# Optimization experiments

Measured on AMD Instinct MI355X. Metric: run time of the kernel, lower is better.

## Reference

```python
import jax, jax.numpy as jnp
import numpy as np

N_AGENTS = 8
N_ACTIONS = 16
SAMPLE = 16
STATE_DIM = 256
EMBED = 256
IN_DIM = N_AGENTS * N_ACTIONS + STATE_DIM  # 384


def setup_inputs() -> dict:
    key = jax.random.key(0)
    ks = jax.random.split(key, 12)
    bs, t = 32, 32
    s = 0.05
    return {
        "states": jax.random.normal(ks[0], (bs, t, STATE_DIM), jnp.float32),
        "agent_qs": jax.random.normal(ks[1], (bs, t, N_AGENTS, N_ACTIONS), jnp.float32),
        "W1": jax.random.normal(ks[2], (IN_DIM, EMBED), jnp.float32) * s,
        "b1": jnp.zeros((EMBED,), jnp.float32),
        "W2": jax.random.normal(ks[3], (EMBED, EMBED), jnp.float32) * s,
        "b2": jnp.zeros((EMBED,), jnp.float32),
        "W3": jax.random.normal(ks[4], (EMBED, 1), jnp.float32) * s,
        "b3": jnp.zeros((1,), jnp.float32),
        "Vw1": jax.random.normal(ks[5], (STATE_DIM, EMBED), jnp.float32) * s,
        "Vb1": jnp.zeros((EMBED,), jnp.float32),
        "Vw2": jax.random.normal(ks[6], (EMBED, 1), jnp.float32) * s,
        "Vb2": jnp.zeros((1,), jnp.float32),
    }


def reference(states, agent_qs, W1, b1, W2, b2, W3, b3, Vw1, Vb1, Vw2, Vb2):
    bs, t = states.shape[0], states.shape[1]
    B = bs * t
    A, NA, S, sd = N_AGENTS, N_ACTIONS, SAMPLE, STATE_DIM
    st = states.reshape(B, sd)
    qs = agent_qs.reshape(B, A, NA)

    # --- sample grand coalitions (random permutation per (B,S) row) ---
    perm_key = jax.random.key(42)
    u = jax.random.uniform(perm_key, (B, S, A))
    pos = jnp.argsort(u, axis=-1)          # grand_coalitions_pos: agent i -> position pos[i]
    inv = jnp.argsort(pos, axis=-1)        # grand_coalitions: position j -> agent inv[j]

    indiv = jax.nn.one_hot(pos, A, dtype=st.dtype)                         # (B,S,A,A)
    subcoal = (jnp.arange(A)[None, None, None, :] <= pos[..., None]).astype(st.dtype)
    no_i = subcoal - indiv                                                 # coalition members excl. self

    # reorder agent qs along position dim: reordered[b,s,j,:] = qs[b, inv[b,s,j], :]
    reordered = jnp.take_along_axis(
        jnp.broadcast_to(qs[:, None], (B, S, A, NA)), inv[..., None], axis=2)

    # (B,S,A,A,NA): detach contribution of other coalition members
    coal = (jax.lax.stop_gradient(reordered[:, :, None] * no_i[..., None])
            + reordered[:, :, None] * indiv[..., None])

    x = coal.reshape(B * S * A, A * NA)
    stx = jnp.broadcast_to(st[:, None, None], (B, S, A, sd)).reshape(B * S * A, sd)
    inp = jnp.concatenate([stx, x], axis=1)

    h = jax.nn.relu(inp @ W1 + b1)
    h = jax.nn.relu(h @ W2 + b2)
    advs = h @ W3 + b3
    v = jax.nn.relu(stx @ Vw1 + Vb1) @ Vw2 + Vb2

    marginal = (advs + v).reshape(B, S, A)
    shapley = marginal.mean(axis=1)        # mean over samples
    return shapley.reshape(bs, t, A)
```

## Files before the change

kernel.cpp:

```cpp
#include <hip/hip_runtime.h>


#define A_N   8
#define NA_N  16
#define S_N   16
#define SD    256
#define EMB   256
#define B_TOT 1024

typedef __bf16 bf16x8 __attribute__((ext_vector_type(8)));
typedef float  f32x4  __attribute__((ext_vector_type(4)));

__device__ __forceinline__ f32x4 splat4(float v) {
  f32x4 x; x[0] = v; x[1] = v; x[2] = v; x[3] = v; return x;
}
__device__ __forceinline__ bf16x8 zero8() {
  bf16x8 z;
#pragma unroll
  for (int j = 0; j < 8; ++j) z[j] = (__bf16)0.0f;
  return z;
}

__device__ __forceinline__ float jax_uniform(unsigned idx) {
  const unsigned ks0 = 0u, ks1 = 42u, ks2 = 0x1BD11BDAu ^ 42u;
  unsigned x0 = 0u + ks0;
  unsigned x1 = idx + ks1;
#define TF_RND(r) { x0 += x1; x1 = (x1 << (r)) | (x1 >> (32 - (r))); x1 ^= x0; }
  TF_RND(13) TF_RND(15) TF_RND(26) TF_RND(6)  x0 += ks1; x1 += ks2 + 1u;
  TF_RND(17) TF_RND(29) TF_RND(16) TF_RND(24) x0 += ks2; x1 += ks0 + 2u;
  TF_RND(13) TF_RND(15) TF_RND(26) TF_RND(6)  x0 += ks0; x1 += ks1 + 3u;
  TF_RND(17) TF_RND(29) TF_RND(16) TF_RND(24) x0 += ks1; x1 += ks2 + 4u;
  TF_RND(13) TF_RND(15) TF_RND(26) TF_RND(6)  x0 += ks2; x1 += ks0 + 5u;
#undef TF_RND
  const unsigned bits = x0 ^ x1;
  return __uint_as_float((bits >> 9) | 0x3F800000u) - 1.0f;
}

__global__ __launch_bounds__(256) void prep_pack_kernel(
    const float* __restrict__ states, const float* __restrict__ W1,
    const float* __restrict__ b1, const float* __restrict__ Vw1,
    const float* __restrict__ Vb1, const float* __restrict__ Vw2,
    const float* __restrict__ Vb2, const float* __restrict__ W2,
    float* __restrict__ sW, float* __restrict__ vout,
    __bf16* __restrict__ W1b_bf, __bf16* __restrict__ W2_bf) {
  __shared__ float st_l[2][SD];
  __shared__ float red_l[2][4];

  if (blockIdx.x >= 512) {
    const int ts = (blockIdx.x - 512) * 256 + threadIdx.x;
    if (ts < 4096) {
      const int t = ts >> 10, rem = ts & 1023, u = rem >> 6, Lp = rem & 63;
      const int qp = Lp >> 4, l15p = Lp & 15;
#pragma unroll
      for (int j = 0; j < 8; ++j) {
        const int k = t * 32 + qp * 8 + j, nn = u * 16 + l15p;
        W1b_bf[ts * 8 + j] = (__bf16)W1[(SD + k) * EMB + nn];
      }
    } else {
      const int ts2 = ts - 4096;
      const int t = ts2 >> 10, rem = ts2 & 1023, u = rem >> 6, Lp = rem & 63;
      const int qp = Lp >> 4, l15p = Lp & 15;
#pragma unroll
      for (int j = 0; j < 8; ++j) {
        const int k = t * 32 + qp * 8 + j, nn = u * 16 + l15p;
        W2_bf[ts2 * 8 + j] = (__bf16)W2[k * EMB + nn];
      }
    }
    return;
  }

  const int b0 = blockIdx.x * 2;
  const int n = threadIdx.x;

#pragma unroll
  for (int i = 0; i < 2; ++i) st_l[i][n] = states[(b0 + i) * SD + n];
  __syncthreads();

  float aS[2], aV[2];
  const float b1n = b1[n], vb1n = Vb1[n];
#pragma unroll
  for (int i = 0; i < 2; ++i) { aS[i] = b1n; aV[i] = vb1n; }

#pragma unroll 8
  for (int k = 0; k < SD; ++k) {
    const float wv = W1[k * EMB + n];
    const float vw = Vw1[k * EMB + n];
#pragma unroll
    for (int i = 0; i < 2; ++i) {
      const float s = st_l[i][k];
      aS[i] = fmaf(s, wv, aS[i]);
      aV[i] = fmaf(s, vw, aV[i]);
    }
  }
#pragma unroll
  for (int i = 0; i < 2; ++i) sW[(b0 + i) * EMB + n] = aS[i];

  const float vw2 = Vw2[n];
#pragma unroll
  for (int i = 0; i < 2; ++i) {
    float c = fmaxf(aV[i], 0.f) * vw2;
#pragma unroll
    for (int off = 32; off; off >>= 1) c += __shfl_down(c, off);
    if ((n & 63) == 0) red_l[i][n >> 6] = c;
  }
  __syncthreads();
  if (n < 2)
    vout[b0 + n] = red_l[n][0] + red_l[n][1] + red_l[n][2] + red_l[n][3] + Vb2[0];
}

__global__ __launch_bounds__(256, 4) void main_kernel(
    const float* __restrict__ agent_qs, const float* __restrict__ b2g,
    const float* __restrict__ W3, const float* __restrict__ b3,
    const float* __restrict__ sW, const float* __restrict__ vv,
    const __bf16* __restrict__ W1b_bf, const __bf16* __restrict__ W2_bf,
    float* __restrict__ out) {
  __shared__ bf16x8 h1_l[32 * 64];
  __shared__ __attribute__((aligned(16))) __bf16 qs_bf[A_N * NA_N];
  __shared__ float u_l[128];
  __shared__ int   inv_l[128];
  __shared__ int   pos_l[128];
  __shared__ float adv_part[4][64];
  __shared__ float marg_l[128];

  const int b = blockIdx.x;
  const int n = threadIdx.x;
  const int w = n >> 6, L = n & 63, q = L >> 4, l15 = L & 15;
  const int s7 = l15 & 7;
  const int sl = l15 >> 3;
  const int jq = q >> 1;
  const int na0 = (q & 1) * 8;
  const int Lsw = L ^ ((L >> 3) & 3);

  if (n < 128) {
    qs_bf[n] = (__bf16)agent_qs[b * 128 + n];
    u_l[n] = jax_uniform((unsigned)(b * 128 + n));
  }
  __syncthreads();

  if (n < 128) {
    const int s = n >> 3, a = n & 7;
    const float u = u_l[n];
    int r = 0;
#pragma unroll
    for (int a2 = 0; a2 < A_N; ++a2) {
      const float u2 = u_l[s * 8 + a2];
      r += (u2 < u || (u2 == u && a2 < a)) ? 1 : 0;
    }
    inv_l[n] = r;
    pos_l[s * 8 + r] = a;
  }
  __syncthreads();

  const bool diag_on = (jq <= sl);

#pragma unroll 1
  for (int p = 0; p < 2; ++p) {
    const int invbase = (p * 8 + s7) * 8;

#pragma unroll 1
    for (int nh = 0; nh < 2; ++nh) {
      f32x4 acc[4][2];
#pragma unroll
      for (int i = 0; i < 2; ++i) {
        const float sv = sW[b * EMB + (w * 4 + nh * 2 + i) * 16 + l15];
#pragma unroll
        for (int mt = 0; mt < 4; ++mt) acc[mt][i] = splat4(sv);
      }
#pragma unroll
      for (int t = 0; t < 4; ++t) {
        const int ag = inv_l[invbase + 2 * t + jq];
        const bf16x8 afb = *(const bf16x8*)&qs_bf[ag * NA_N + na0];
        const bf16x8 afd = diag_on ? afb : zero8();
        bf16x8 bfr[2];
#pragma unroll
        for (int i = 0; i < 2; ++i)
          bfr[i] = *(const bf16x8*)
              &W1b_bf[((t * 16 + w * 4 + nh * 2 + i) * 64 + L) * 8];
#pragma unroll
        for (int mt = 0; mt < 4; ++mt) {
          if (mt < t) continue;
#pragma unroll
          for (int i = 0; i < 2; ++i)
            acc[mt][i] = __builtin_amdgcn_mfma_f32_16x16x32_bf16(
                (mt == t) ? afd : afb, bfr[i], acc[mt][i], 0, 0, 0);
        }
      }
      __bf16* h1e = (__bf16*)h1_l;
#pragma unroll
      for (int i = 0; i < 2; ++i) {
        const int X = w * 4 + nh * 2 + i;
        const int hi = (X & 1) * 2 + sl;
        const int xr = (q >> 1) | ((hi & 1) << 1);
#pragma unroll
        for (int mt = 0; mt < 4; ++mt) {
          const int ub = ((X >> 1) * 4 + mt) * 64 + (hi << 4);
#pragma unroll
          for (int r = 0; r < 4; ++r) {
            const float v = fmaxf(acc[mt][i][r], 0.f);
            const int u = ub + ((q * 4 + r) ^ xr);
            h1e[u * 8 + s7] = (__bf16)v;
          }
        }
      }
    }
    __syncthreads();

    float psum[4][4];
#pragma unroll
    for (int mt = 0; mt < 4; ++mt)
#pragma unroll
      for (int r = 0; r < 4; ++r) psum[mt][r] = 0.f;

#pragma unroll 1
    for (int nh = 0; nh < 2; ++nh) {
      f32x4 acc[4][2];
#pragma unroll
      for (int i = 0; i < 2; ++i) {
        const float bv = b2g[(w * 4 + nh * 2 + i) * 16 + l15];
#pragma unroll
        for (int mt = 0; mt < 4; ++mt) acc[mt][i] = splat4(bv);
      }
#pragma unroll 2
      for (int t = 0; t < 8; ++t) {
        bf16x8 bfr[2];
#pragma unroll
        for (int i = 0; i < 2; ++i)
          bfr[i] = *(const bf16x8*)
              &W2_bf[((t * 16 + w * 4 + nh * 2 + i) * 64 + L) * 8];
#pragma unroll
        for (int mt = 0; mt < 4; ++mt) {
          const bf16x8 af = h1_l[(t * 4 + mt) * 64 + Lsw];
#pragma unroll
          for (int i = 0; i < 2; ++i)
            acc[mt][i] = __builtin_amdgcn_mfma_f32_16x16x32_bf16(
                af, bfr[i], acc[mt][i], 0, 0, 0);
        }
      }
#pragma unroll
      for (int i = 0; i < 2; ++i) {
        const float w3v = W3[(w * 4 + nh * 2 + i) * 16 + l15];
#pragma unroll
        for (int mt = 0; mt < 4; ++mt)
#pragma unroll
          for (int r = 0; r < 4; ++r)
            psum[mt][r] = fmaf(fmaxf(acc[mt][i][r], 0.f), w3v, psum[mt][r]);
      }
    }

#pragma unroll
    for (int mt = 0; mt < 4; ++mt) {
#pragma unroll
      for (int r = 0; r < 4; ++r) {
        float sum = psum[mt][r];
#pragma unroll
        for (int off = 1; off < 16; off <<= 1) sum += __shfl_xor(sum, off);
        if (l15 == 0) adv_part[w][mt * 16 + q * 4 + r] = sum;
      }
    }
    __syncthreads();
    if (n < 64)
      marg_l[p * 64 + n] = adv_part[0][n] + adv_part[1][n] +
                           adv_part[2][n] + adv_part[3][n];
    __syncthreads();
  }

  if (n < A_N) {
    float sh = 0.f;
#pragma unroll
    for (int s = 0; s < S_N; ++s) {
      const int pr = pos_l[s * 8 + n];
      sh += marg_l[((s >> 3) << 6) + pr * 8 + (s & 7)];
    }
    out[b * A_N + n] = sh * (1.f / 16.f) + b3[0] + vv[b];
  }
}

extern "C" void kernel_launch(void* const* d_in, const int* in_sizes, int n_in,
                              void* d_out, int out_size, void* d_ws,
                              size_t ws_size, hipStream_t stream) {
  const float* states   = (const float*)d_in[0];
  const float* agent_qs = (const float*)d_in[1];
  const float* W1       = (const float*)d_in[2];
  const float* b1       = (const float*)d_in[3];
  const float* W2       = (const float*)d_in[4];
  const float* b2       = (const float*)d_in[5];
  const float* W3       = (const float*)d_in[6];
  const float* b3       = (const float*)d_in[7];
  const float* Vw1      = (const float*)d_in[8];
  const float* Vb1      = (const float*)d_in[9];
  const float* Vw2      = (const float*)d_in[10];
  const float* Vb2      = (const float*)d_in[11];
  float* out = (float*)d_out;

  char* ws = (char*)d_ws;
  float*  sW     = (float*)(ws);
  float*  vv     = (float*)(ws + 1048576);
  __bf16* W1b_bf = (__bf16*)(ws + 1052672);
  __bf16* W2_bf  = (__bf16*)(ws + 1118208);

  prep_pack_kernel<<<560, 256, 0, stream>>>(states, W1, b1, Vw1, Vb1, Vw2,
                                            Vb2, W2, sW, vv, W1b_bf, W2_bf);
  main_kernel<<<B_TOT, 256, 0, stream>>>(agent_qs, b2, W3, b3, sW, vv,
                                         W1b_bf, W2_bf, out);
}
```

Measured before the change: 117.2 us.

## Compute full layer-2 N-tile per wave in one pass; batch four states per prep block

The layer-2 MFMA loop now keeps all four output column tiles per wave in 16 accumulators. This replaces the two sequential halves, so each LDS A-fragment is loaded once per t instead of twice. To make room for the extra accumulator registers, the main kernel's occupancy hint drops from 4 to 3 blocks per CU. The prep kernel now processes four state rows per block instead of two, which halves how often the W1/Vw1 weights are re-read, at the cost of fewer blocks.

```diff
diff --git a/kernel.cpp b/kernel.cpp
--- a/kernel.cpp
+++ b/kernel.cpp
@@ -43,11 +43,11 @@
     const float* __restrict__ Vb2, const float* __restrict__ W2,
     float* __restrict__ sW, float* __restrict__ vout,
     __bf16* __restrict__ W1b_bf, __bf16* __restrict__ W2_bf) {
-  __shared__ float st_l[2][SD];
-  __shared__ float red_l[2][4];
-
-  if (blockIdx.x >= 512) {
-    const int ts = (blockIdx.x - 512) * 256 + threadIdx.x;
+  __shared__ float st_l[4][SD];
+  __shared__ float red_l[4][4];
+
+  if (blockIdx.x >= 256) {
+    const int ts = (blockIdx.x - 256) * 256 + threadIdx.x;
     if (ts < 4096) {
       const int t = ts >> 10, rem = ts & 1023, u = rem >> 6, Lp = rem & 63;
       const int qp = Lp >> 4, l15p = Lp & 15;
@@ -69,46 +69,46 @@
     return;
   }
 
-  const int b0 = blockIdx.x * 2;
+  const int b0 = blockIdx.x * 4;
   const int n = threadIdx.x;
 
 #pragma unroll
-  for (int i = 0; i < 2; ++i) st_l[i][n] = states[(b0 + i) * SD + n];
+  for (int i = 0; i < 4; ++i) st_l[i][n] = states[(b0 + i) * SD + n];
   __syncthreads();
 
-  float aS[2], aV[2];
+  float aS[4], aV[4];
   const float b1n = b1[n], vb1n = Vb1[n];
 #pragma unroll
-  for (int i = 0; i < 2; ++i) { aS[i] = b1n; aV[i] = vb1n; }
+  for (int i = 0; i < 4; ++i) { aS[i] = b1n; aV[i] = vb1n; }
 
 #pragma unroll 8
   for (int k = 0; k < SD; ++k) {
     const float wv = W1[k * EMB + n];
     const float vw = Vw1[k * EMB + n];
 #pragma unroll
-    for (int i = 0; i < 2; ++i) {
+    for (int i = 0; i < 4; ++i) {
       const float s = st_l[i][k];
       aS[i] = fmaf(s, wv, aS[i]);
       aV[i] = fmaf(s, vw, aV[i]);
     }
   }
 #pragma unroll
-  for (int i = 0; i < 2; ++i) sW[(b0 + i) * EMB + n] = aS[i];
+  for (int i = 0; i < 4; ++i) sW[(b0 + i) * EMB + n] = aS[i];
 
   const float vw2 = Vw2[n];
 #pragma unroll
-  for (int i = 0; i < 2; ++i) {
+  for (int i = 0; i < 4; ++i) {
     float c = fmaxf(aV[i], 0.f) * vw2;
 #pragma unroll
     for (int off = 32; off; off >>= 1) c += __shfl_down(c, off);
     if ((n & 63) == 0) red_l[i][n >> 6] = c;
   }
   __syncthreads();
-  if (n < 2)
+  if (n < 4)
     vout[b0 + n] = red_l[n][0] + red_l[n][1] + red_l[n][2] + red_l[n][3] + Vb2[0];
 }
 
-__global__ __launch_bounds__(256, 4) void main_kernel(
+__global__ __launch_bounds__(256, 3) void main_kernel(
     const float* __restrict__ agent_qs, const float* __restrict__ b2g,
     const float* __restrict__ W3, const float* __restrict__ b3,
     const float* __restrict__ sW, const float* __restrict__ vv,
@@ -205,46 +205,42 @@
     }
     __syncthreads();
 
+    f32x4 acc2[4][4];
+#pragma unroll
+    for (int c = 0; c < 4; ++c) {
+      const float bv = b2g[(w * 4 + c) * 16 + l15];
+#pragma unroll
+      for (int mt = 0; mt < 4; ++mt) acc2[mt][c] = splat4(bv);
+    }
+#pragma unroll 2
+    for (int t = 0; t < 8; ++t) {
+      bf16x8 af[4];
+#pragma unroll
+      for (int mt = 0; mt < 4; ++mt) af[mt] = h1_l[(t * 4 + mt) * 64 + Lsw];
+#pragma unroll
+      for (int c = 0; c < 4; ++c) {
+        const bf16x8 bfr = *(const bf16x8*)
+            &W2_bf[((t * 16 + w * 4 + c) * 64 + L) * 8];
+#pragma unroll
+        for (int mt = 0; mt < 4; ++mt)
+          acc2[mt][c] = __builtin_amdgcn_mfma_f32_16x16x32_bf16(
+              af[mt], bfr, acc2[mt][c], 0, 0, 0);
+      }
+    }
+
     float psum[4][4];
 #pragma unroll
     for (int mt = 0; mt < 4; ++mt)
 #pragma unroll
       for (int r = 0; r < 4; ++r) psum[mt][r] = 0.f;
-
-#pragma unroll 1
-    for (int nh = 0; nh < 2; ++nh) {
-      f32x4 acc[4][2];
-#pragma unroll
-      for (int i = 0; i < 2; ++i) {
-        const float bv = b2g[(w * 4 + nh * 2 + i) * 16 + l15];
-#pragma unroll
-        for (int mt = 0; mt < 4; ++mt) acc[mt][i] = splat4(bv);
-      }
-#pragma unroll 2
-      for (int t = 0; t < 8; ++t) {
-        bf16x8 bfr[2];
-#pragma unroll
-        for (int i = 0; i < 2; ++i)
-          bfr[i] = *(const bf16x8*)
-              &W2_bf[((t * 16 + w * 4 + nh * 2 + i) * 64 + L) * 8];
-#pragma unroll
-        for (int mt = 0; mt < 4; ++mt) {
-          const bf16x8 af = h1_l[(t * 4 + mt) * 64 + Lsw];
-#pragma unroll
-          for (int i = 0; i < 2; ++i)
-            acc[mt][i] = __builtin_amdgcn_mfma_f32_16x16x32_bf16(
-                af, bfr[i], acc[mt][i], 0, 0, 0);
-        }
-      }
-#pragma unroll
-      for (int i = 0; i < 2; ++i) {
-        const float w3v = W3[(w * 4 + nh * 2 + i) * 16 + l15];
-#pragma unroll
-        for (int mt = 0; mt < 4; ++mt)
-#pragma unroll
-          for (int r = 0; r < 4; ++r)
-            psum[mt][r] = fmaf(fmaxf(acc[mt][i][r], 0.f), w3v, psum[mt][r]);
-      }
+#pragma unroll
+    for (int c = 0; c < 4; ++c) {
+      const float w3v = W3[(w * 4 + c) * 16 + l15];
+#pragma unroll
+      for (int mt = 0; mt < 4; ++mt)
+#pragma unroll
+        for (int r = 0; r < 4; ++r)
+          psum[mt][r] = fmaf(fmaxf(acc2[mt][c][r], 0.f), w3v, psum[mt][r]);
     }
 
 #pragma unroll
@@ -298,7 +294,7 @@
   __bf16* W1b_bf = (__bf16*)(ws + 1052672);
   __bf16* W2_bf  = (__bf16*)(ws + 1118208);
 
-  prep_pack_kernel<<<560, 256, 0, stream>>>(states, W1, b1, Vw1, Vb1, Vw2,
+  prep_pack_kernel<<<304, 256, 0, stream>>>(states, W1, b1, Vw1, Vb1, Vw2,
                                             Vb2, W2, sW, vv, W1b_bf, W2_bf);
   main_kernel<<<B_TOT, 256, 0, stream>>>(agent_qs, b2, W3, b3, sW, vv,
                                          W1b_bf, W2_bf, out);
```

Result: slower. 126.8 us (+8.2%).

## Split state projection K-range across block groups and batch four rows per block

Applied to the files above, without the earlier changes.

The prep kernel's state projection is restructured so each block handles four batch rows instead of two. The W1 K-dimension is split between two block groups, one doing k<128 plus the full value head and the other doing k>=128, with partial results in separate buffers. The main kernel sums the two partials when initialising its accumulators. This aims to balance per-block work and reuse weight loads across more rows, at the cost of an extra global buffer and an extra load per accumulator init. The value-head blocks still do more work than the other group, so the load stays uneven.

```diff
diff --git a/kernel.cpp b/kernel.cpp
--- a/kernel.cpp
+++ b/kernel.cpp
@@ -41,10 +41,11 @@
     const float* __restrict__ b1, const float* __restrict__ Vw1,
     const float* __restrict__ Vb1, const float* __restrict__ Vw2,
     const float* __restrict__ Vb2, const float* __restrict__ W2,
-    float* __restrict__ sW, float* __restrict__ vout,
+    float* __restrict__ sWa, float* __restrict__ sWb,
+    float* __restrict__ vout,
     __bf16* __restrict__ W1b_bf, __bf16* __restrict__ W2_bf) {
-  __shared__ float st_l[2][SD];
-  __shared__ float red_l[2][4];
+  __shared__ float st_l[4][SD];
+  __shared__ float red_l[4][4];
 
   if (blockIdx.x >= 512) {
     const int ts = (blockIdx.x - 512) * 256 + threadIdx.x;
@@ -69,49 +70,73 @@
     return;
   }
 
-  const int b0 = blockIdx.x * 2;
+  const bool isA = (blockIdx.x < 256);
+  const int g = isA ? blockIdx.x : blockIdx.x - 256;
+  const int b0 = g * 4;
   const int n = threadIdx.x;
 
 #pragma unroll
-  for (int i = 0; i < 2; ++i) st_l[i][n] = states[(b0 + i) * SD + n];
+  for (int i = 0; i < 4; ++i) st_l[i][n] = states[(b0 + i) * SD + n];
   __syncthreads();
 
-  float aS[2], aV[2];
-  const float b1n = b1[n], vb1n = Vb1[n];
-#pragma unroll
-  for (int i = 0; i < 2; ++i) { aS[i] = b1n; aV[i] = vb1n; }
+  if (isA) {
+    float aS[4], aV[4];
+    const float b1n = b1[n], vb1n = Vb1[n];
+#pragma unroll
+    for (int i = 0; i < 4; ++i) { aS[i] = b1n; aV[i] = vb1n; }
 
 #pragma unroll 8
-  for (int k = 0; k < SD; ++k) {
-    const float wv = W1[k * EMB + n];
-    const float vw = Vw1[k * EMB + n];
-#pragma unroll
-    for (int i = 0; i < 2; ++i) {
-      const float s = st_l[i][k];
-      aS[i] = fmaf(s, wv, aS[i]);
-      aV[i] = fmaf(s, vw, aV[i]);
-    }
-  }
-#pragma unroll
-  for (int i = 0; i < 2; ++i) sW[(b0 + i) * EMB + n] = aS[i];
-
-  const float vw2 = Vw2[n];
-#pragma unroll
-  for (int i = 0; i < 2; ++i) {
-    float c = fmaxf(aV[i], 0.f) * vw2;
-#pragma unroll
-    for (int off = 32; off; off >>= 1) c += __shfl_down(c, off);
-    if ((n & 63) == 0) red_l[i][n >> 6] = c;
-  }
-  __syncthreads();
-  if (n < 2)
-    vout[b0 + n] = red_l[n][0] + red_l[n][1] + red_l[n][2] + red_l[n][3] + Vb2[0];
+    for (int k = 0; k < 128; ++k) {
+      const float wv = W1[k * EMB + n];
+      const float vw = Vw1[k * EMB + n];
+#pragma unroll
+      for (int i = 0; i < 4; ++i) {
+        const float s = st_l[i][k];
+        aS[i] = fmaf(s, wv, aS[i]);
+        aV[i] = fmaf(s, vw, aV[i]);
+      }
+    }
+#pragma unroll 8
+    for (int k = 128; k < SD; ++k) {
+      const float vw = Vw1[k * EMB + n];
+#pragma unroll
+      for (int i = 0; i < 4; ++i) aV[i] = fmaf(st_l[i][k], vw, aV[i]);
+    }
+#pragma unroll
+    for (int i = 0; i < 4; ++i) sWa[(b0 + i) * EMB + n] = aS[i];
+
+    const float vw2 = Vw2[n];
+#pragma unroll
+    for (int i = 0; i < 4; ++i) {
+      float c = fmaxf(aV[i], 0.f) * vw2;
+#pragma unroll
+      for (int off = 32; off; off >>= 1) c += __shfl_down(c, off);
+      if ((n & 63) == 0) red_l[i][n >> 6] = c;
+    }
+    __syncthreads();
+    if (n < 4)
+      vout[b0 + n] =
+          red_l[n][0] + red_l[n][1] + red_l[n][2] + red_l[n][3] + Vb2[0];
+  } else {
+    float aS[4];
+#pragma unroll
+    for (int i = 0; i < 4; ++i) aS[i] = 0.f;
+#pragma unroll 8
+    for (int k = 128; k < SD; ++k) {
+      const float wv = W1[k * EMB + n];
+#pragma unroll
+      for (int i = 0; i < 4; ++i) aS[i] = fmaf(st_l[i][k], wv, aS[i]);
+    }
+#pragma unroll
+    for (int i = 0; i < 4; ++i) sWb[(b0 + i) * EMB + n] = aS[i];
+  }
 }
 
 __global__ __launch_bounds__(256, 4) void main_kernel(
     const float* __restrict__ agent_qs, const float* __restrict__ b2g,
     const float* __restrict__ W3, const float* __restrict__ b3,
-    const float* __restrict__ sW, const float* __restrict__ vv,
+    const float* __restrict__ sWa, const float* __restrict__ sWb,
+    const float* __restrict__ vv,
     const __bf16* __restrict__ W1b_bf, const __bf16* __restrict__ W2_bf,
     float* __restrict__ out) {
   __shared__ bf16x8 h1_l[32 * 64];
@@ -162,7 +187,8 @@
       f32x4 acc[4][2];
 #pragma unroll
       for (int i = 0; i < 2; ++i) {
-        const float sv = sW[b * EMB + (w * 4 + nh * 2 + i) * 16 + l15];
+        const int col = (w * 4 + nh * 2 + i) * 16 + l15;
+        const float sv = sWa[b * EMB + col] + sWb[b * EMB + col];
 #pragma unroll
         for (int mt = 0; mt < 4; ++mt) acc[mt][i] = splat4(sv);
       }
@@ -293,13 +319,15 @@
   float* out = (float*)d_out;
 
   char* ws = (char*)d_ws;
-  float*  sW     = (float*)(ws);
-  float*  vv     = (float*)(ws + 1048576);
-  __bf16* W1b_bf = (__bf16*)(ws + 1052672);
-  __bf16* W2_bf  = (__bf16*)(ws + 1118208);
+  float*  sWa    = (float*)(ws);
+  float*  sWb    = (float*)(ws + 1048576);
+  float*  vv     = (float*)(ws + 2097152);
+  __bf16* W1b_bf = (__bf16*)(ws + 2101248);
+  __bf16* W2_bf  = (__bf16*)(ws + 2166784);
 
   prep_pack_kernel<<<560, 256, 0, stream>>>(states, W1, b1, Vw1, Vb1, Vw2,
-                                            Vb2, W2, sW, vv, W1b_bf, W2_bf);
-  main_kernel<<<B_TOT, 256, 0, stream>>>(agent_qs, b2, W3, b3, sW, vv,
+                                            Vb2, W2, sWa, sWb, vv,
+                                            W1b_bf, W2_bf);
+  main_kernel<<<B_TOT, 256, 0, stream>>>(agent_qs, b2, W3, b3, sWa, sWb, vv,
                                          W1b_bf, W2_bf, out);
 }
```

Result: no change. 118.4 us (+1.0%).

## Process all 16 samples in one pass with wider M tiles per block

Applied to the files above, without the earlier changes.

Removes the outer two-pass loop over sample halves. All 128 rows (16 samples x 8 positions) are now computed in a single pass with 8 M-tiles per wave. Each W1/W2 B-fragment load from global memory now feeds twice as many MFMAs, and the per-pass syncs and reductions are dropped. In exchange the h1 LDS buffer doubles, register pressure rises sharply (acc2 is 8x4 f32x4 tiles), and launch bounds fall to 2 blocks per CU, which lowers occupancy. The row-to-sample mapping and LDS swizzle are rewritten to match.

```diff
diff --git a/kernel.cpp b/kernel.cpp
--- a/kernel.cpp
+++ b/kernel.cpp
@@ -108,28 +108,28 @@
     vout[b0 + n] = red_l[n][0] + red_l[n][1] + red_l[n][2] + red_l[n][3] + Vb2[0];
 }
 
-__global__ __launch_bounds__(256, 4) void main_kernel(
+__global__ __launch_bounds__(256, 2) void main_kernel(
     const float* __restrict__ agent_qs, const float* __restrict__ b2g,
     const float* __restrict__ W3, const float* __restrict__ b3,
     const float* __restrict__ sW, const float* __restrict__ vv,
     const __bf16* __restrict__ W1b_bf, const __bf16* __restrict__ W2_bf,
     float* __restrict__ out) {
-  __shared__ bf16x8 h1_l[32 * 64];
+  __shared__ bf16x8 h1_l[64 * 64];
   __shared__ __attribute__((aligned(16))) __bf16 qs_bf[A_N * NA_N];
   __shared__ float u_l[128];
   __shared__ int   inv_l[128];
   __shared__ int   pos_l[128];
-  __shared__ float adv_part[4][64];
+  __shared__ float adv_part[4][128];
   __shared__ float marg_l[128];
 
   const int b = blockIdx.x;
   const int n = threadIdx.x;
   const int w = n >> 6, L = n & 63, q = L >> 4, l15 = L & 15;
-  const int s7 = l15 & 7;
-  const int sl = l15 >> 3;
   const int jq = q >> 1;
   const int na0 = (q & 1) * 8;
-  const int Lsw = L ^ ((L >> 3) & 3);
+  const int xmask = ((q >> 1) << 1) | ((l15 >> 3) << 2);
+  const int Lr = q * 16 + l15;
+  const int Lswz = Lr ^ (((Lr >> 3) & 3) << 1);
 
   if (n < 128) {
     qs_bf[n] = (__bf16)agent_qs[b * 128 + n];
@@ -151,125 +151,115 @@
   }
   __syncthreads();
 
-  const bool diag_on = (jq <= sl);
-
 #pragma unroll 1
-  for (int p = 0; p < 2; ++p) {
-    const int invbase = (p * 8 + s7) * 8;
-
-#pragma unroll 1
-    for (int nh = 0; nh < 2; ++nh) {
-      f32x4 acc[4][2];
-#pragma unroll
-      for (int i = 0; i < 2; ++i) {
-        const float sv = sW[b * EMB + (w * 4 + nh * 2 + i) * 16 + l15];
-#pragma unroll
-        for (int mt = 0; mt < 4; ++mt) acc[mt][i] = splat4(sv);
-      }
-#pragma unroll
-      for (int t = 0; t < 4; ++t) {
-        const int ag = inv_l[invbase + 2 * t + jq];
-        const bf16x8 afb = *(const bf16x8*)&qs_bf[ag * NA_N + na0];
-        const bf16x8 afd = diag_on ? afb : zero8();
-        bf16x8 bfr[2];
+  for (int nh = 0; nh < 2; ++nh) {
+    f32x4 acc[8][2];
+#pragma unroll
+    for (int i = 0; i < 2; ++i) {
+      const float sv = sW[b * EMB + (w * 4 + nh * 2 + i) * 16 + l15];
+#pragma unroll
+      for (int mt = 0; mt < 8; ++mt) acc[mt][i] = splat4(sv);
+    }
+#pragma unroll
+    for (int t = 0; t < 4; ++t) {
+      const int ag = inv_l[l15 * 8 + 2 * t + jq];
+      const bf16x8 afb = *(const bf16x8*)&qs_bf[ag * NA_N + na0];
+      const bf16x8 af0 = (jq == 0) ? afb : zero8();
+      bf16x8 bfr[2];
+#pragma unroll
+      for (int i = 0; i < 2; ++i)
+        bfr[i] = *(const bf16x8*)
+            &W1b_bf[((t * 16 + w * 4 + nh * 2 + i) * 64 + L) * 8];
+#pragma unroll
+      for (int mt = 0; mt < 8; ++mt) {
+        if (mt < 2 * t) continue;
 #pragma unroll
         for (int i = 0; i < 2; ++i)
-          bfr[i] = *(const bf16x8*)
-              &W1b_bf[((t * 16 + w * 4 + nh * 2 + i) * 64 + L) * 8];
-#pragma unroll
-        for (int mt = 0; mt < 4; ++mt) {
-          if (mt < t) continue;
-#pragma unroll
-          for (int i = 0; i < 2; ++i)
-            acc[mt][i] = __builtin_amdgcn_mfma_f32_16x16x32_bf16(
-                (mt == t) ? afd : afb, bfr[i], acc[mt][i], 0, 0, 0);
-        }
-      }
+          acc[mt][i] = __builtin_amdgcn_mfma_f32_16x16x32_bf16(
+              (mt == 2 * t) ? af0 : afb, bfr[i], acc[mt][i], 0, 0, 0);
+      }
+    }
+    {
       __bf16* h1e = (__bf16*)h1_l;
 #pragma unroll
       for (int i = 0; i < 2; ++i) {
         const int X = w * 4 + nh * 2 + i;
-        const int hi = (X & 1) * 2 + sl;
-        const int xr = (q >> 1) | ((hi & 1) << 1);
-#pragma unroll
-        for (int mt = 0; mt < 4; ++mt) {
-          const int ub = ((X >> 1) * 4 + mt) * 64 + (hi << 4);
+        const int ubase = ((X >> 1) * 8) * 64 + ((X & 1) * 2 + (l15 >> 3)) * 16;
+        const int j7 = l15 & 7;
+#pragma unroll
+        for (int mt = 0; mt < 8; ++mt) {
 #pragma unroll
           for (int r = 0; r < 4; ++r) {
             const float v = fmaxf(acc[mt][i][r], 0.f);
-            const int u = ub + ((q * 4 + r) ^ xr);
-            h1e[u * 8 + s7] = (__bf16)v;
+            const int u = ubase + mt * 64 + ((q * 4 + r) ^ xmask);
+            h1e[u * 8 + j7] = (__bf16)v;
           }
         }
       }
     }
-    __syncthreads();
-
-    float psum[4][4];
-#pragma unroll
-    for (int mt = 0; mt < 4; ++mt)
-#pragma unroll
-      for (int r = 0; r < 4; ++r) psum[mt][r] = 0.f;
-
+  }
+  __syncthreads();
+
+  f32x4 acc2[8][4];
+#pragma unroll
+  for (int c = 0; c < 4; ++c) {
+    const float bv = b2g[(w * 4 + c) * 16 + l15];
+#pragma unroll
+    for (int mt = 0; mt < 8; ++mt) acc2[mt][c] = splat4(bv);
+  }
 #pragma unroll 1
-    for (int nh = 0; nh < 2; ++nh) {
-      f32x4 acc[4][2];
-#pragma unroll
-      for (int i = 0; i < 2; ++i) {
-        const float bv = b2g[(w * 4 + nh * 2 + i) * 16 + l15];
-#pragma unroll
-        for (int mt = 0; mt < 4; ++mt) acc[mt][i] = splat4(bv);
-      }
-#pragma unroll 2
-      for (int t = 0; t < 8; ++t) {
-        bf16x8 bfr[2];
-#pragma unroll
-        for (int i = 0; i < 2; ++i)
-          bfr[i] = *(const bf16x8*)
-              &W2_bf[((t * 16 + w * 4 + nh * 2 + i) * 64 + L) * 8];
-#pragma unroll
-        for (int mt = 0; mt < 4; ++mt) {
-          const bf16x8 af = h1_l[(t * 4 + mt) * 64 + Lsw];
-#pragma unroll
-          for (int i = 0; i < 2; ++i)
-            acc[mt][i] = __builtin_amdgcn_mfma_f32_16x16x32_bf16(
-                af, bfr[i], acc[mt][i], 0, 0, 0);
-        }
-      }
-#pragma unroll
-      for (int i = 0; i < 2; ++i) {
-        const float w3v = W3[(w * 4 + nh * 2 + i) * 16 + l15];
-#pragma unroll
-        for (int mt = 0; mt < 4; ++mt)
-#pragma unroll
-          for (int r = 0; r < 4; ++r)
-            psum[mt][r] = fmaf(fmaxf(acc[mt][i][r], 0.f), w3v, psum[mt][r]);
-      }
-    }
-
-#pragma unroll
-    for (int mt = 0; mt < 4; ++mt) {
-#pragma unroll
-      for (int r = 0; r < 4; ++r) {
-        float sum = psum[mt][r];
-#pragma unroll
-        for (int off = 1; off < 16; off <<= 1) sum += __shfl_xor(sum, off);
-        if (l15 == 0) adv_part[w][mt * 16 + q * 4 + r] = sum;
-      }
-    }
-    __syncthreads();
-    if (n < 64)
-      marg_l[p * 64 + n] = adv_part[0][n] + adv_part[1][n] +
-                           adv_part[2][n] + adv_part[3][n];
-    __syncthreads();
-  }
+  for (int t = 0; t < 8; ++t) {
+    bf16x8 af[8];
+#pragma unroll
+    for (int mt = 0; mt < 8; ++mt) af[mt] = h1_l[(t * 8 + mt) * 64 + Lswz];
+#pragma unroll
+    for (int c = 0; c < 4; ++c) {
+      const bf16x8 bfr = *(const bf16x8*)
+          &W2_bf[((t * 16 + w * 4 + c) * 64 + L) * 8];
+#pragma unroll
+      for (int mt = 0; mt < 8; ++mt)
+        acc2[mt][c] = __builtin_amdgcn_mfma_f32_16x16x32_bf16(
+            af[mt], bfr, acc2[mt][c], 0, 0, 0);
+    }
+  }
+
+  float psum[8][4];
+#pragma unroll
+  for (int mt = 0; mt < 8; ++mt)
+#pragma unroll
+    for (int r = 0; r < 4; ++r) psum[mt][r] = 0.f;
+#pragma unroll
+  for (int c = 0; c < 4; ++c) {
+    const float w3v = W3[(w * 4 + c) * 16 + l15];
+#pragma unroll
+    for (int mt = 0; mt < 8; ++mt)
+#pragma unroll
+      for (int r = 0; r < 4; ++r)
+        psum[mt][r] = fmaf(fmaxf(acc2[mt][c][r], 0.f), w3v, psum[mt][r]);
+  }
+
+#pragma unroll
+  for (int mt = 0; mt < 8; ++mt) {
+#pragma unroll
+    for (int r = 0; r < 4; ++r) {
+      float sum = psum[mt][r];
+#pragma unroll
+      for (int off = 1; off < 16; off <<= 1) sum += __shfl_xor(sum, off);
+      if (l15 == 0) adv_part[w][mt * 16 + q * 4 + r] = sum;
+    }
+  }
+  __syncthreads();
+  if (n < 128)
+    marg_l[n] = adv_part[0][n] + adv_part[1][n] +
+                adv_part[2][n] + adv_part[3][n];
+  __syncthreads();
 
   if (n < A_N) {
     float sh = 0.f;
 #pragma unroll
     for (int s = 0; s < S_N; ++s) {
       const int pr = pos_l[s * 8 + n];
-      sh += marg_l[((s >> 3) << 6) + pr * 8 + (s & 7)];
+      sh += marg_l[pr * 16 + s];
     }
     out[b * A_N + n] = sh * (1.f / 16.f) + b3[0] + vv[b];
   }
```

Result: slower. 123.0 us (+4.9%).
